# Optimization experiments

Measured on AMD Instinct MI355X. Metric: run time of the kernel, lower is better.

## Reference

```python
import jax, jax.numpy as jnp
import numpy as np

WIN = (7, 7)
NUM_HEADS = 6
DIM = 192
NW = 64          # windows per image
BATCH = 64       # images
B_ = BATCH * NW  # 4096 window-batches
N = WIN[0] * WIN[1]  # 49


def _relative_position_index():
    ch, cw = np.arange(WIN[0]), np.arange(WIN[1])
    coords = np.stack(np.meshgrid(ch, cw, indexing='ij'))          # [2, Wh, Ww]
    cf = coords.reshape(2, -1)                                      # [2, N]
    rel = cf[:, :, None] - cf[:, None, :]                           # [2, N, N]
    rel = rel.transpose(1, 2, 0).astype(np.int64)                   # [N, N, 2]
    rel[:, :, 0] += WIN[0] - 1
    rel[:, :, 1] += WIN[1] - 1
    rel[:, :, 0] *= 2 * WIN[1] - 1
    return rel.sum(-1).astype(np.int32)                             # [N, N]


def setup_inputs() -> dict:
    key = jax.random.key(0)
    ks = jax.random.split(key, 8)
    x = jax.random.normal(ks[0], (B_, N, DIM), dtype=jnp.float32)
    # additive shift-window mask: 0 where allowed, -100 where disallowed
    u = jax.random.uniform(ks[1], (NW, N, N))
    attn_mask = jnp.where(u < 0.15, -100.0, 0.0).astype(jnp.float32)
    rpb_table = jax.random.normal(ks[2], ((2 * WIN[0] - 1) * (2 * WIN[1] - 1), NUM_HEADS), dtype=jnp.float32) * 0.02
    rel_index = jnp.asarray(_relative_position_index())
    std = 1.0 / np.sqrt(DIM)
    qkv_w = jax.random.normal(ks[3], (3 * DIM, DIM), dtype=jnp.float32) * std
    qkv_b = jax.random.normal(ks[4], (3 * DIM,), dtype=jnp.float32) * 0.02
    proj_w = jax.random.normal(ks[5], (DIM, DIM), dtype=jnp.float32) * std
    proj_b = jax.random.normal(ks[6], (DIM,), dtype=jnp.float32) * 0.02
    return {"x": x, "attn_mask": attn_mask, "rpb_table": rpb_table,
            "rel_index": rel_index, "qkv_w": qkv_w, "qkv_b": qkv_b,
            "proj_w": proj_w, "proj_b": proj_b}


def reference(x, attn_mask, rpb_table, rel_index, qkv_w, qkv_b, proj_w, proj_b):
    Bw, n, C = x.shape
    H = NUM_HEADS
    hd = C // H
    scale = hd ** -0.5
    # qkv projection: [Bw, N, 3, H, hd] -> (3, Bw, H, N, hd)
    qkv = (x @ qkv_w.T + qkv_b).reshape(Bw, n, 3, H, hd).transpose(2, 0, 3, 1, 4)
    q, k, v = qkv[0], qkv[1], qkv[2]
    # gathered relative position bias: [H, N, N]
    rel_bias = rpb_table[rel_index.reshape(-1)].reshape(n, n, H).transpose(2, 0, 1)
    # scores [Bw, H, N, N]
    attn = jnp.einsum('bhnd,bhmd->bhnm', q * scale, k) + rel_bias[None]
    nW = attn_mask.shape[0]
    attn = attn.reshape(Bw // nW, nW, H, n, n) + attn_mask[None, :, None]
    attn = jax.nn.softmax(attn.reshape(Bw, H, n, n), axis=-1)
    out = jnp.einsum('bhnm,bhmd->bhnd', attn, v)  # [Bw, H, N, hd]
    out = out.transpose(0, 2, 1, 3).reshape(Bw, n, C)
    return out @ proj_w.T + proj_b
```

## Files before the change

### kernel.cpp

```cpp
#include <hip/hip_runtime.h>
#include <stdint.h>

typedef unsigned short ushort_t;
typedef __attribute__((ext_vector_type(8))) short bf16x8;
typedef __attribute__((ext_vector_type(4))) float f32x4;
typedef __attribute__((ext_vector_type(4))) unsigned int u32x4;

#define NTOK 49
#define DIMC 192
#define NH 6
#define HD 32
#define SCALE 0.17677669529663687f
#define XS 200
#define VTS 72
#define PS 72
#define MS 66
#define RS 68

#define OFF_X    0
#define OFF_Q    25600
#define OFF_K    51200
#define OFF_VT   76800
#define OFF_P    104448
#define OFF_MASK 122880
#define OFF_RPB  139776
#define OFF_REL  145184
#define OFF_BQ   153888
#define OFF_BP   156192
#define SMEM_BYTES 156960

#define QKVW_N (576 * 192)
#define PROJW_N (192 * 192)
#define QKV_GRP (4 * 9 * 6 * 64)
#define PROJ_GRP (4 * 3 * 6 * 64)
#define WBF_BYTES ((QKVW_N + PROJW_N) * 2)
#define BIAS_FLOATS (64 * 6 * 4 * 4 * 4 * 16 * 4)
#define WS_NEED1 ((size_t)WBF_BYTES)
#define WS_NEED2 ((size_t)WBF_BYTES + (size_t)BIAS_FLOATS * 4)

__device__ __forceinline__ ushort_t f2bf(float f) {
    uint32_t x = __builtin_bit_cast(uint32_t, f);
    x += 0x7fffu + ((x >> 16) & 1u);
    return (ushort_t)(x >> 16);
}

__device__ __forceinline__ bf16x8 cvt8(const float* p) {
    f32x4 a = *(const f32x4*)p;
    f32x4 b = *(const f32x4*)(p + 4);
    bf16x8 r;
    r[0] = (short)f2bf(a[0]); r[1] = (short)f2bf(a[1]);
    r[2] = (short)f2bf(a[2]); r[3] = (short)f2bf(a[3]);
    r[4] = (short)f2bf(b[0]); r[5] = (short)f2bf(b[1]);
    r[6] = (short)f2bf(b[2]); r[7] = (short)f2bf(b[3]);
    return r;
}

__global__ __launch_bounds__(256) void swz_weights_kernel(
    const float* __restrict__ qkvw, const float* __restrict__ projw,
    ushort_t* __restrict__ dst)
{
    int i = blockIdx.x * 256 + threadIdx.x;
    if (i >= QKV_GRP + PROJ_GRP) return;
    const float* src;
    float s = 1.0f;
    if (i < QKV_GRP) {
        int lane = i & 63, t = i >> 6;
        int kk = t % 6, nt = (t / 6) % 9, cq = t / 54;
        int col = cq * 144 + nt * 16 + (lane & 15);
        int k0 = kk * 32 + (lane >> 4) * 8;
        src = qkvw + col * DIMC + k0;
        if (col < 192) s = SCALE;
    } else {
        int j = i - QKV_GRP;
        int lane = j & 63, t = j >> 6;
        int kk = t % 6, nt = (t / 6) % 3, cq = t / 18;
        int col = cq * 48 + nt * 16 + (lane & 15);
        int k0 = kk * 32 + (lane >> 4) * 8;
        src = projw + col * DIMC + k0;
    }
    f32x4 a = *(const f32x4*)src;
    f32x4 b = *(const f32x4*)(src + 4);
    u32x4 o;
    o[0] = (uint32_t)f2bf(a[0] * s) | ((uint32_t)f2bf(a[1] * s) << 16);
    o[1] = (uint32_t)f2bf(a[2] * s) | ((uint32_t)f2bf(a[3] * s) << 16);
    o[2] = (uint32_t)f2bf(b[0] * s) | ((uint32_t)f2bf(b[1] * s) << 16);
    o[3] = (uint32_t)f2bf(b[2] * s) | ((uint32_t)f2bf(b[3] * s) << 16);
    *(u32x4*)(dst + (size_t)i * 8) = o;
}

__global__ __launch_bounds__(256) void bias_kernel(
    const float* __restrict__ mask_g, const float* __restrict__ rpb_g,
    const int* __restrict__ rel_g, float* __restrict__ dst)
{
    int i = blockIdx.x * 256 + threadIdx.x;
    if (i >= BIAS_FLOATS / 4) return;
    int c = i & 15, g = (i >> 4) & 3, t = (i >> 6) & 3, wsid = (i >> 8) & 3;
    int hw = i >> 10;
    int h = hw % 6, wi = hw / 6;
    int m0 = 16 * wsid + 4 * g, n = 16 * t + c;
    f32x4 v;
    #pragma unroll
    for (int r = 0; r < 4; ++r) {
        int m = m0 + r;
        float val;
        if (n >= NTOK)      val = -30000.0f;
        else if (m >= NTOK) val = 0.0f;
        else val = mask_g[(size_t)wi * (NTOK * NTOK) + m * NTOK + n]
                 + rpb_g[(size_t)rel_g[m * NTOK + n] * NH + h];
        v[r] = val;
    }
    *(f32x4*)(dst + (size_t)i * 4) = v;
}

template <int MODE>
__global__ __launch_bounds__(512, 2) void win_attn_kernel(
    const float* __restrict__ x_g,
    const float* __restrict__ mask_g,
    const float* __restrict__ rpb_g,
    const int* __restrict__ rel_g,
    const float* __restrict__ qkvw_g,
    const float* __restrict__ qkvb_g,
    const float* __restrict__ projw_g,
    const float* __restrict__ projb_g,
    const ushort_t* __restrict__ wbf_g,
    const float* __restrict__ bias_g,
    float* __restrict__ out_g)
{
    extern __shared__ char smem[];
    ushort_t* x_lds  = (ushort_t*)(smem + OFF_X);
    ushort_t* q_lds  = (ushort_t*)(smem + OFF_Q);
    ushort_t* k_lds  = (ushort_t*)(smem + OFF_K);
    ushort_t* vT     = (ushort_t*)(smem + OFF_VT);
    ushort_t* P_lds  = (ushort_t*)(smem + OFF_P);
    float*    mask_p = (float*)(smem + OFF_MASK);
    float*    rpb_l  = (float*)(smem + OFF_RPB);
    ushort_t* rel_p  = (ushort_t*)(smem + OFF_REL);
    float*    bq     = (float*)(smem + OFF_BQ);
    float*    bp     = (float*)(smem + OFF_BP);

    const int tid  = threadIdx.x;
    const int b    = blockIdx.x;
    const int wi   = b & 63;
    const int w    = tid >> 6;
    const int lane = tid & 63;
    const int g    = lane >> 4;
    const int c    = lane & 15;

    {
        const float* xg = x_g + (size_t)b * (NTOK * DIMC);
        for (int i = tid; i < 64 * 24; i += 512) {
            int row = i / 24, col = (i % 24) * 8;
            u32x4 v = {0u, 0u, 0u, 0u};
            if (row < NTOK) {
                const float* src = xg + row * DIMC + col;
                f32x4 a = *(const f32x4*)src;
                f32x4 d = *(const f32x4*)(src + 4);
                v[0] = (uint32_t)f2bf(a[0]) | ((uint32_t)f2bf(a[1]) << 16);
                v[1] = (uint32_t)f2bf(a[2]) | ((uint32_t)f2bf(a[3]) << 16);
                v[2] = (uint32_t)f2bf(d[0]) | ((uint32_t)f2bf(d[1]) << 16);
                v[3] = (uint32_t)f2bf(d[2]) | ((uint32_t)f2bf(d[3]) << 16);
            }
            *(u32x4*)&x_lds[row * XS + col] = v;
        }
        if constexpr (MODE < 2) {
            const float* mw = mask_g + (size_t)wi * (NTOK * NTOK);
            for (int i = tid; i < 64 * 64; i += 512) {
                int m = i >> 6, n = i & 63;
                float f;
                if (n >= NTOK)      f = -30000.0f;
                else if (m >= NTOK) f = 0.0f;
                else                f = mw[m * NTOK + n];
                mask_p[m * MS + n] = f;
                rel_p[m * RS + n] = (m < NTOK && n < NTOK) ? (ushort_t)rel_g[m * NTOK + n]
                                                           : (ushort_t)0;
            }
            for (int i = tid; i < 169 * 6; i += 512)
                rpb_l[(i / 6) * 8 + (i % 6)] = rpb_g[i];
        }
        for (int i = tid; i < 576; i += 512) {
            float v = qkvb_g[i];
            if constexpr (MODE == 2) { if (i < 192) v *= SCALE; }
            bq[i] = v;
        }
        if (tid < 192) bp[tid] = projb_g[tid];
    }
    __syncthreads();

    {
        const int mh = w >> 2, cq = w & 3;
        const ushort_t* wq = wbf_g + (size_t)cq * (9 * 6 * 64 * 8);

        bf16x8 ring[4][6];
        if constexpr (MODE >= 1) {
            #pragma unroll
            for (int p = 0; p < 3; ++p)
                #pragma unroll
                for (int kk = 0; kk < 6; ++kk)
                    ring[p][kk] = *(const bf16x8*)(wq + (size_t)((p * 6 + kk) * 64 + lane) * 8);
            __builtin_amdgcn_sched_barrier(0);
        }

        bf16x8 ax[2][6];
        #pragma unroll
        for (int mt = 0; mt < 2; ++mt)
            #pragma unroll
            for (int kk = 0; kk < 6; ++kk)
                ax[mt][kk] = *(const bf16x8*)&x_lds[(32 * mh + 16 * mt + c) * XS + kk * 32 + g * 8];

        #pragma unroll
        for (int nt = 0; nt < 9; ++nt) {
            const int cg = 144 * cq + nt * 16 + c;
            bf16x8 bw[6];
            if constexpr (MODE >= 1) {
                if (nt + 3 < 9) {
                    #pragma unroll
                    for (int kk = 0; kk < 6; ++kk)
                        ring[(nt + 3) & 3][kk] =
                            *(const bf16x8*)(wq + (size_t)(((nt + 3) * 6 + kk) * 64 + lane) * 8);
                }
                __builtin_amdgcn_sched_barrier(0);
                #pragma unroll
                for (int kk = 0; kk < 6; ++kk) bw[kk] = ring[nt & 3][kk];
            } else {
                #pragma unroll
                for (int kk = 0; kk < 6; ++kk)
                    bw[kk] = cvt8(qkvw_g + (size_t)cg * DIMC + kk * 32 + g * 8);
            }
            f32x4 z = {0.f, 0.f, 0.f, 0.f};
            f32x4 acc[2] = {z, z};
            #pragma unroll
            for (int kk = 0; kk < 6; ++kk)
                #pragma unroll
                for (int mt = 0; mt < 2; ++mt)
                    acc[mt] = __builtin_amdgcn_mfma_f32_16x16x32_bf16(ax[mt][kk], bw[kk], acc[mt], 0, 0, 0);

            const float bias = bq[cg];
            const int seg = 144 * cq + nt * 16;
            if (seg < 192) {
                #pragma unroll
                for (int mt = 0; mt < 2; ++mt)
                    #pragma unroll
                    for (int r = 0; r < 4; ++r)
                        q_lds[(32 * mh + 16 * mt + g * 4 + r) * XS + cg] = f2bf(acc[mt][r] + bias);
            } else if (seg < 384) {
                const int ck = cg - 192;
                #pragma unroll
                for (int mt = 0; mt < 2; ++mt)
                    #pragma unroll
                    for (int r = 0; r < 4; ++r)
                        k_lds[(32 * mh + 16 * mt + g * 4 + r) * XS + ck] = f2bf(acc[mt][r] + bias);
            } else {
                const int cv = cg - 384;
                #pragma unroll
                for (int mt = 0; mt < 2; ++mt) {
                    uint32_t lo = (uint32_t)f2bf(acc[mt][0] + bias) | ((uint32_t)f2bf(acc[mt][1] + bias) << 16);
                    uint32_t hi = (uint32_t)f2bf(acc[mt][2] + bias) | ((uint32_t)f2bf(acc[mt][3] + bias) << 16);
                    uint32_t* dst = (uint32_t*)&vT[cv * VTS + 32 * mh + 16 * mt + g * 4];
                    dst[0] = lo; dst[1] = hi;
                }
            }
        }
    }
    __syncthreads();

    bf16x8 pw[3][6];
    {
        const int wsid = w & 3, hh = w >> 2;
        ushort_t* Pw = P_lds + w * (16 * PS);
        const int mq0 = 16 * wsid + g * 4;

        auto head = [&](int h) {
            bf16x8 aq = *(const bf16x8*)&q_lds[(16 * wsid + c) * XS + h * HD + g * 8];
            f32x4 S[4];
            if constexpr (MODE == 2) {
                const float* bC = bias_g + ((size_t)((wi * 6 + h) * 4 + wsid) * 4) * 256 + lane * 4;
                #pragma unroll
                for (int t = 0; t < 4; ++t) {
                    f32x4 Ct = *(const f32x4*)(bC + t * 256);
                    bf16x8 bk = *(const bf16x8*)&k_lds[(16 * t + c) * XS + h * HD + g * 8];
                    S[t] = __builtin_amdgcn_mfma_f32_16x16x32_bf16(aq, bk, Ct, 0, 0, 0);
                }
            } else {
                #pragma unroll
                for (int t = 0; t < 4; ++t) {
                    bf16x8 bk = *(const bf16x8*)&k_lds[(16 * t + c) * XS + h * HD + g * 8];
                    f32x4 z = {0.f, 0.f, 0.f, 0.f};
                    S[t] = __builtin_amdgcn_mfma_f32_16x16x32_bf16(aq, bk, z, 0, 0, 0);
                }
            }
            float rinv[4];
            #pragma unroll
            for (int r = 0; r < 4; ++r) {
                float sv[4];
                if constexpr (MODE == 2) {
                    #pragma unroll
                    for (int t = 0; t < 4; ++t) sv[t] = S[t][r];
                } else {
                    const int mq = mq0 + r;
                    const float*    mrow = mask_p + mq * MS;
                    const ushort_t* rrow = rel_p + mq * RS;
                    #pragma unroll
                    for (int t = 0; t < 4; ++t) {
                        const int n = 16 * t + c;
                        sv[t] = S[t][r] * SCALE + rpb_l[(int)rrow[n] * 8 + h] + mrow[n];
                    }
                }
                float vmax = fmaxf(fmaxf(sv[0], sv[1]), fmaxf(sv[2], sv[3]));
                #pragma unroll
                for (int xm = 1; xm < 16; xm <<= 1)
                    vmax = fmaxf(vmax, __shfl_xor(vmax, xm));
                float sum = 0.f;
                float ev[4];
                #pragma unroll
                for (int t = 0; t < 4; ++t) {
                    ev[t] = __expf(fmaxf(sv[t] - vmax, -80.0f));
                    sum += ev[t];
                }
                #pragma unroll
                for (int xm = 1; xm < 16; xm <<= 1)
                    sum += __shfl_xor(sum, xm);
                rinv[r] = 1.0f / sum;
                #pragma unroll
                for (int t = 0; t < 4; ++t)
                    Pw[(g * 4 + r) * PS + 16 * t + c] = f2bf(ev[t]);
            }
            f32x4 z = {0.f, 0.f, 0.f, 0.f};
            f32x4 O[2] = {z, z};
            #pragma unroll
            for (int ks = 0; ks < 2; ++ks) {
                bf16x8 ap = *(const bf16x8*)&Pw[c * PS + ks * 32 + g * 8];
                #pragma unroll
                for (int nt = 0; nt < 2; ++nt) {
                    bf16x8 bv = *(const bf16x8*)&vT[(h * HD + nt * 16 + c) * VTS + ks * 32 + g * 8];
                    O[nt] = __builtin_amdgcn_mfma_f32_16x16x32_bf16(ap, bv, O[nt], 0, 0, 0);
                }
            }
            #pragma unroll
            for (int nt = 0; nt < 2; ++nt)
                #pragma unroll
                for (int r = 0; r < 4; ++r)
                    x_lds[(16 * wsid + g * 4 + r) * XS + h * HD + nt * 16 + c] =
                        f2bf(O[nt][r] * rinv[r]);
        };

        head(hh * 3 + 0);
        head(hh * 3 + 1);
        if constexpr (MODE >= 1) {
            const int cq4 = w & 3;
            const ushort_t* wp = wbf_g + QKVW_N + (size_t)cq4 * (3 * 6 * 64 * 8);
            #pragma unroll
            for (int nt = 0; nt < 3; ++nt)
                #pragma unroll
                for (int kk = 0; kk < 6; ++kk)
                    pw[nt][kk] = *(const bf16x8*)(wp + (size_t)((nt * 6 + kk) * 64 + lane) * 8);
            __builtin_amdgcn_sched_barrier(0);
        }
        head(hh * 3 + 2);
    }
    __syncthreads();

    {
        const int mh = w >> 2, cq4 = w & 3;
        bf16x8 aa[2][6];
        #pragma unroll
        for (int mt = 0; mt < 2; ++mt)
            #pragma unroll
            for (int kk = 0; kk < 6; ++kk)
                aa[mt][kk] = *(const bf16x8*)&x_lds[(32 * mh + 16 * mt + c) * XS + kk * 32 + g * 8];

        float* og = out_g + (size_t)b * (NTOK * DIMC);
        #pragma unroll
        for (int nt = 0; nt < 3; ++nt) {
            const int cg = 48 * cq4 + nt * 16 + c;
            bf16x8 bw[6];
            #pragma unroll
            for (int kk = 0; kk < 6; ++kk) {
                if constexpr (MODE >= 1)
                    bw[kk] = pw[nt][kk];
                else
                    bw[kk] = cvt8(projw_g + (size_t)cg * DIMC + kk * 32 + g * 8);
            }
            f32x4 z = {0.f, 0.f, 0.f, 0.f};
            f32x4 acc[2] = {z, z};
            #pragma unroll
            for (int kk = 0; kk < 6; ++kk)
                #pragma unroll
                for (int mt = 0; mt < 2; ++mt)
                    acc[mt] = __builtin_amdgcn_mfma_f32_16x16x32_bf16(aa[mt][kk], bw[kk], acc[mt], 0, 0, 0);
            const float bias = bp[cg];
            #pragma unroll
            for (int mt = 0; mt < 2; ++mt)
                #pragma unroll
                for (int r = 0; r < 4; ++r) {
                    const int row = 32 * mh + 16 * mt + g * 4 + r;
                    if (row < NTOK) og[row * DIMC + cg] = acc[mt][r] + bias;
                }
        }
    }
}

extern "C" void kernel_launch(void* const* d_in, const int* in_sizes, int n_in,
                              void* d_out, int out_size, void* d_ws, size_t ws_size,
                              hipStream_t stream) {
    (void)in_sizes; (void)n_in; (void)out_size;
    const float* x_g     = (const float*)d_in[0];
    const float* mask_g  = (const float*)d_in[1];
    const float* rpb_g   = (const float*)d_in[2];
    const int*   rel_g   = (const int*)d_in[3];
    const float* qkvw_g  = (const float*)d_in[4];
    const float* qkvb_g  = (const float*)d_in[5];
    const float* projw_g = (const float*)d_in[6];
    const float* projb_g = (const float*)d_in[7];
    float*       out_g   = (float*)d_out;

    const bool has_w = (d_ws != nullptr) && (ws_size >= WS_NEED1);
    const bool has_b = (d_ws != nullptr) && (ws_size >= WS_NEED2);
    ushort_t* wbf = (ushort_t*)d_ws;
    float* bias4 = (float*)((char*)d_ws + WBF_BYTES);

    if (has_w) {
        int ngrp = QKV_GRP + PROJ_GRP;
        hipLaunchKernelGGL(swz_weights_kernel, dim3((ngrp + 255) / 256), dim3(256), 0, stream,
                           qkvw_g, projw_g, wbf);
    }
    if (has_b) {
        int nthr = BIAS_FLOATS / 4;
        hipLaunchKernelGGL(bias_kernel, dim3((nthr + 255) / 256), dim3(256), 0, stream,
                           mask_g, rpb_g, rel_g, bias4);
        hipFuncSetAttribute((const void*)win_attn_kernel<2>,
                            hipFuncAttributeMaxDynamicSharedMemorySize, SMEM_BYTES);
        hipLaunchKernelGGL(win_attn_kernel<2>, dim3(4096), dim3(512), SMEM_BYTES, stream,
                           x_g, mask_g, rpb_g, rel_g, qkvw_g, qkvb_g, projw_g, projb_g,
                           wbf, bias4, out_g);
    } else if (has_w) {
        hipFuncSetAttribute((const void*)win_attn_kernel<1>,
                            hipFuncAttributeMaxDynamicSharedMemorySize, SMEM_BYTES);
        hipLaunchKernelGGL(win_attn_kernel<1>, dim3(4096), dim3(512), SMEM_BYTES, stream,
                           x_g, mask_g, rpb_g, rel_g, qkvw_g, qkvb_g, projw_g, projb_g,
                           wbf, (const float*)nullptr, out_g);
    } else {
        hipFuncSetAttribute((const void*)win_attn_kernel<0>,
                            hipFuncAttributeMaxDynamicSharedMemorySize, SMEM_BYTES);
        hipLaunchKernelGGL(win_attn_kernel<0>, dim3(4096), dim3(512), SMEM_BYTES, stream,
                           x_g, mask_g, rpb_g, rel_g, qkvw_g, qkvb_g, projw_g, projb_g,
                           (const ushort_t*)nullptr, (const float*)nullptr, out_g);
    }
}
```

Before: 249.9 us.

## Process two windows per block with prefetched next-window x in registers

Each block now handles two consecutive windows, with the grid halved. The second window's x is loaded into registers during the first window and written to a second LDS buffer after attention, so that load overlaps compute. Projection weights are loaded once and reused for both windows. Biases are folded into the MFMA accumulator init, and conversions use packed v_cvt_pk_bf16_f32. The cost is fewer blocks in flight, more register pressure, and an LDS region shared with mask/rpb buffers.

```diff
diff --git a/kernel.cpp b/kernel.cpp
--- a/kernel.cpp
+++ b/kernel.cpp
@@ -16,17 +16,19 @@
 #define PS 72
 #define MS 66
 #define RS 68
+#define NWIN 2
 
 #define OFF_X    0
 #define OFF_Q    25600
 #define OFF_K    51200
 #define OFF_VT   76800
 #define OFF_P    104448
-#define OFF_MASK 122880
-#define OFF_RPB  139776
-#define OFF_REL  145184
-#define OFF_BQ   153888
-#define OFF_BP   156192
+#define OFF_BQ   122880
+#define OFF_BP   125184
+#define OFF_X1   125952
+#define OFF_MASK 125952
+#define OFF_RPB  142848
+#define OFF_REL  148256
 #define SMEM_BYTES 156960
 
 #define QKVW_N (576 * 192)
@@ -42,6 +44,11 @@
     uint32_t x = __builtin_bit_cast(uint32_t, f);
     x += 0x7fffu + ((x >> 16) & 1u);
     return (ushort_t)(x >> 16);
+}
+__device__ __forceinline__ uint32_t cvtpk(float lo, float hi) {
+    uint32_t r;
+    asm("v_cvt_pk_bf16_f32 %0, %1, %2" : "=v"(r) : "v"(lo), "v"(hi));
+    return r;
 }
 
 __device__ __forceinline__ bf16x8 cvt8(const float* p) {
@@ -128,6 +135,7 @@
 {
     extern __shared__ char smem[];
     ushort_t* x_lds  = (ushort_t*)(smem + OFF_X);
+    ushort_t* x1_lds = (ushort_t*)(smem + OFF_X1);
     ushort_t* q_lds  = (ushort_t*)(smem + OFF_Q);
     ushort_t* k_lds  = (ushort_t*)(smem + OFF_K);
     ushort_t* vT     = (ushort_t*)(smem + OFF_VT);
@@ -139,15 +147,14 @@
     float*    bp     = (float*)(smem + OFF_BP);
 
     const int tid  = threadIdx.x;
-    const int b    = blockIdx.x;
-    const int wi   = b & 63;
+    const int blk  = blockIdx.x;
     const int w    = tid >> 6;
     const int lane = tid & 63;
     const int g    = lane >> 4;
     const int c    = lane & 15;
 
-    {
-        const float* xg = x_g + (size_t)b * (NTOK * DIMC);
+    auto stage_x = [&](int bb, ushort_t* dst) {
+        const float* xg = x_g + (size_t)bb * (NTOK * DIMC);
         for (int i = tid; i < 64 * 24; i += 512) {
             int row = i / 24, col = (i % 24) * 8;
             u32x4 v = {0u, 0u, 0u, 0u};
@@ -155,246 +162,308 @@
                 const float* src = xg + row * DIMC + col;
                 f32x4 a = *(const f32x4*)src;
                 f32x4 d = *(const f32x4*)(src + 4);
-                v[0] = (uint32_t)f2bf(a[0]) | ((uint32_t)f2bf(a[1]) << 16);
-                v[1] = (uint32_t)f2bf(a[2]) | ((uint32_t)f2bf(a[3]) << 16);
-                v[2] = (uint32_t)f2bf(d[0]) | ((uint32_t)f2bf(d[1]) << 16);
-                v[3] = (uint32_t)f2bf(d[2]) | ((uint32_t)f2bf(d[3]) << 16);
-            }
-            *(u32x4*)&x_lds[row * XS + col] = v;
+                v[0] = cvtpk(a[0], a[1]); v[1] = cvtpk(a[2], a[3]);
+                v[2] = cvtpk(d[0], d[1]); v[3] = cvtpk(d[2], d[3]);
+            }
+            *(u32x4*)&dst[row * XS + col] = v;
         }
-        if constexpr (MODE < 2) {
-            const float* mw = mask_g + (size_t)wi * (NTOK * NTOK);
-            for (int i = tid; i < 64 * 64; i += 512) {
-                int m = i >> 6, n = i & 63;
-                float f;
-                if (n >= NTOK)      f = -30000.0f;
-                else if (m >= NTOK) f = 0.0f;
-                else                f = mw[m * NTOK + n];
-                mask_p[m * MS + n] = f;
-                rel_p[m * RS + n] = (m < NTOK && n < NTOK) ? (ushort_t)rel_g[m * NTOK + n]
-                                                           : (ushort_t)0;
-            }
-            for (int i = tid; i < 169 * 6; i += 512)
-                rpb_l[(i / 6) * 8 + (i % 6)] = rpb_g[i];
+    };
+    auto stage_aux = [&](int wi) {
+        const float* mw = mask_g + (size_t)wi * (NTOK * NTOK);
+        for (int i = tid; i < 64 * 64; i += 512) {
+            int m = i >> 6, n = i & 63;
+            float f;
+            if (n >= NTOK)      f = -30000.0f;
+            else if (m >= NTOK) f = 0.0f;
+            else                f = mw[m * NTOK + n];
+            mask_p[m * MS + n] = f;
+            rel_p[m * RS + n] = (m < NTOK && n < NTOK) ? (ushort_t)rel_g[m * NTOK + n]
+                                                       : (ushort_t)0;
         }
-        for (int i = tid; i < 576; i += 512) {
-            float v = qkvb_g[i];
-            if constexpr (MODE == 2) { if (i < 192) v *= SCALE; }
-            bq[i] = v;
-        }
-        if (tid < 192) bp[tid] = projb_g[tid];
+        for (int i = tid; i < 169 * 6; i += 512)
+            rpb_l[(i / 6) * 8 + (i % 6)] = rpb_g[i];
+    };
+
+    stage_x(blk * NWIN, x_lds);
+    if constexpr (MODE < 2) stage_aux((blk * NWIN) & 63);
+    for (int i = tid; i < 576; i += 512) {
+        float v = qkvb_g[i];
+        if constexpr (MODE >= 1) { if (i < 192) v *= SCALE; }
+        bq[i] = v;
     }
+    if (tid < 192) bp[tid] = projb_g[tid];
     __syncthreads();
 
-    {
-        const int mh = w >> 2, cq = w & 3;
-        const ushort_t* wq = wbf_g + (size_t)cq * (9 * 6 * 64 * 8);
-
-        bf16x8 ring[4][6];
-        if constexpr (MODE >= 1) {
-            #pragma unroll
-            for (int p = 0; p < 3; ++p)
-                #pragma unroll
-                for (int kk = 0; kk < 6; ++kk)
-                    ring[p][kk] = *(const bf16x8*)(wq + (size_t)((p * 6 + kk) * 64 + lane) * 8);
-            __builtin_amdgcn_sched_barrier(0);
-        }
-
-        bf16x8 ax[2][6];
-        #pragma unroll
-        for (int mt = 0; mt < 2; ++mt)
-            #pragma unroll
-            for (int kk = 0; kk < 6; ++kk)
-                ax[mt][kk] = *(const bf16x8*)&x_lds[(32 * mh + 16 * mt + c) * XS + kk * 32 + g * 8];
-
-        #pragma unroll
-        for (int nt = 0; nt < 9; ++nt) {
-            const int cg = 144 * cq + nt * 16 + c;
-            bf16x8 bw[6];
+    bf16x8 pw[3][6];
+    f32x4 xa0, xa1, xa2, xd0, xd1, xd2;
+
+    #pragma unroll 1
+    for (int wdx = 0; wdx < NWIN; ++wdx) {
+        const int bb = blk * NWIN + wdx;
+        const int wi = bb & 63;
+        ushort_t* xb = (MODE == 2 && (wdx & 1)) ? x1_lds : x_lds;
+
+        {
+            const int mh = w >> 2, cq = w & 3;
+            const ushort_t* wq = wbf_g + (size_t)cq * (9 * 6 * 64 * 8);
+
+            bf16x8 ring[4][6];
             if constexpr (MODE >= 1) {
-                if (nt + 3 < 9) {
+                #pragma unroll
+                for (int p = 0; p < 3; ++p)
                     #pragma unroll
                     for (int kk = 0; kk < 6; ++kk)
-                        ring[(nt + 3) & 3][kk] =
-                            *(const bf16x8*)(wq + (size_t)(((nt + 3) * 6 + kk) * 64 + lane) * 8);
-                }
+                        ring[p][kk] = *(const bf16x8*)(wq + (size_t)((p * 6 + kk) * 64 + lane) * 8);
                 __builtin_amdgcn_sched_barrier(0);
-                #pragma unroll
-                for (int kk = 0; kk < 6; ++kk) bw[kk] = ring[nt & 3][kk];
-            } else {
-                #pragma unroll
-                for (int kk = 0; kk < 6; ++kk)
-                    bw[kk] = cvt8(qkvw_g + (size_t)cg * DIMC + kk * 32 + g * 8);
-            }
-            f32x4 z = {0.f, 0.f, 0.f, 0.f};
-            f32x4 acc[2] = {z, z};
-            #pragma unroll
-            for (int kk = 0; kk < 6; ++kk)
-                #pragma unroll
-                for (int mt = 0; mt < 2; ++mt)
-                    acc[mt] = __builtin_amdgcn_mfma_f32_16x16x32_bf16(ax[mt][kk], bw[kk], acc[mt], 0, 0, 0);
-
-            const float bias = bq[cg];
-            const int seg = 144 * cq + nt * 16;
-            if (seg < 192) {
-                #pragma unroll
-                for (int mt = 0; mt < 2; ++mt)
-                    #pragma unroll
-                    for (int r = 0; r < 4; ++r)
-                        q_lds[(32 * mh + 16 * mt + g * 4 + r) * XS + cg] = f2bf(acc[mt][r] + bias);
-            } else if (seg < 384) {
-                const int ck = cg - 192;
-                #pragma unroll
-                for (int mt = 0; mt < 2; ++mt)
-                    #pragma unroll
-                    for (int r = 0; r < 4; ++r)
-                        k_lds[(32 * mh + 16 * mt + g * 4 + r) * XS + ck] = f2bf(acc[mt][r] + bias);
-            } else {
-                const int cv = cg - 384;
-                #pragma unroll
-                for (int mt = 0; mt < 2; ++mt) {
-                    uint32_t lo = (uint32_t)f2bf(acc[mt][0] + bias) | ((uint32_t)f2bf(acc[mt][1] + bias) << 16);
-                    uint32_t hi = (uint32_t)f2bf(acc[mt][2] + bias) | ((uint32_t)f2bf(acc[mt][3] + bias) << 16);
-                    uint32_t* dst = (uint32_t*)&vT[cv * VTS + 32 * mh + 16 * mt + g * 4];
-                    dst[0] = lo; dst[1] = hi;
-                }
-            }
-        }
-    }
-    __syncthreads();
-
-    bf16x8 pw[3][6];
-    {
-        const int wsid = w & 3, hh = w >> 2;
-        ushort_t* Pw = P_lds + w * (16 * PS);
-        const int mq0 = 16 * wsid + g * 4;
-
-        auto head = [&](int h) {
-            bf16x8 aq = *(const bf16x8*)&q_lds[(16 * wsid + c) * XS + h * HD + g * 8];
-            f32x4 S[4];
-            if constexpr (MODE == 2) {
-                const float* bC = bias_g + ((size_t)((wi * 6 + h) * 4 + wsid) * 4) * 256 + lane * 4;
-                #pragma unroll
-                for (int t = 0; t < 4; ++t) {
-                    f32x4 Ct = *(const f32x4*)(bC + t * 256);
-                    bf16x8 bk = *(const bf16x8*)&k_lds[(16 * t + c) * XS + h * HD + g * 8];
-                    S[t] = __builtin_amdgcn_mfma_f32_16x16x32_bf16(aq, bk, Ct, 0, 0, 0);
-                }
-            } else {
-                #pragma unroll
-                for (int t = 0; t < 4; ++t) {
-                    bf16x8 bk = *(const bf16x8*)&k_lds[(16 * t + c) * XS + h * HD + g * 8];
-                    f32x4 z = {0.f, 0.f, 0.f, 0.f};
-                    S[t] = __builtin_amdgcn_mfma_f32_16x16x32_bf16(aq, bk, z, 0, 0, 0);
-                }
-            }
-            float rinv[4];
-            #pragma unroll
-            for (int r = 0; r < 4; ++r) {
-                float sv[4];
-                if constexpr (MODE == 2) {
-                    #pragma unroll
-                    for (int t = 0; t < 4; ++t) sv[t] = S[t][r];
-                } else {
-                    const int mq = mq0 + r;
-                    const float*    mrow = mask_p + mq * MS;
-                    const ushort_t* rrow = rel_p + mq * RS;
-                    #pragma unroll
-                    for (int t = 0; t < 4; ++t) {
-                        const int n = 16 * t + c;
-                        sv[t] = S[t][r] * SCALE + rpb_l[(int)rrow[n] * 8 + h] + mrow[n];
-                    }
-                }
-                float vmax = fmaxf(fmaxf(sv[0], sv[1]), fmaxf(sv[2], sv[3]));
-                #pragma unroll
-                for (int xm = 1; xm < 16; xm <<= 1)
-                    vmax = fmaxf(vmax, __shfl_xor(vmax, xm));
-                float sum = 0.f;
-                float ev[4];
-                #pragma unroll
-                for (int t = 0; t < 4; ++t) {
-                    ev[t] = __expf(fmaxf(sv[t] - vmax, -80.0f));
-                    sum += ev[t];
-                }
-                #pragma unroll
-                for (int xm = 1; xm < 16; xm <<= 1)
-                    sum += __shfl_xor(sum, xm);
-                rinv[r] = 1.0f / sum;
-                #pragma unroll
-                for (int t = 0; t < 4; ++t)
-                    Pw[(g * 4 + r) * PS + 16 * t + c] = f2bf(ev[t]);
-            }
-            f32x4 z = {0.f, 0.f, 0.f, 0.f};
-            f32x4 O[2] = {z, z};
-            #pragma unroll
-            for (int ks = 0; ks < 2; ++ks) {
-                bf16x8 ap = *(const bf16x8*)&Pw[c * PS + ks * 32 + g * 8];
-                #pragma unroll
-                for (int nt = 0; nt < 2; ++nt) {
-                    bf16x8 bv = *(const bf16x8*)&vT[(h * HD + nt * 16 + c) * VTS + ks * 32 + g * 8];
-                    O[nt] = __builtin_amdgcn_mfma_f32_16x16x32_bf16(ap, bv, O[nt], 0, 0, 0);
-                }
-            }
-            #pragma unroll
-            for (int nt = 0; nt < 2; ++nt)
-                #pragma unroll
-                for (int r = 0; r < 4; ++r)
-                    x_lds[(16 * wsid + g * 4 + r) * XS + h * HD + nt * 16 + c] =
-                        f2bf(O[nt][r] * rinv[r]);
-        };
-
-        head(hh * 3 + 0);
-        head(hh * 3 + 1);
-        if constexpr (MODE >= 1) {
-            const int cq4 = w & 3;
-            const ushort_t* wp = wbf_g + QKVW_N + (size_t)cq4 * (3 * 6 * 64 * 8);
-            #pragma unroll
-            for (int nt = 0; nt < 3; ++nt)
-                #pragma unroll
-                for (int kk = 0; kk < 6; ++kk)
-                    pw[nt][kk] = *(const bf16x8*)(wp + (size_t)((nt * 6 + kk) * 64 + lane) * 8);
-            __builtin_amdgcn_sched_barrier(0);
-        }
-        head(hh * 3 + 2);
-    }
-    __syncthreads();
-
-    {
-        const int mh = w >> 2, cq4 = w & 3;
-        bf16x8 aa[2][6];
-        #pragma unroll
-        for (int mt = 0; mt < 2; ++mt)
-            #pragma unroll
-            for (int kk = 0; kk < 6; ++kk)
-                aa[mt][kk] = *(const bf16x8*)&x_lds[(32 * mh + 16 * mt + c) * XS + kk * 32 + g * 8];
-
-        float* og = out_g + (size_t)b * (NTOK * DIMC);
-        #pragma unroll
-        for (int nt = 0; nt < 3; ++nt) {
-            const int cg = 48 * cq4 + nt * 16 + c;
-            bf16x8 bw[6];
-            #pragma unroll
-            for (int kk = 0; kk < 6; ++kk) {
-                if constexpr (MODE >= 1)
-                    bw[kk] = pw[nt][kk];
-                else
-                    bw[kk] = cvt8(projw_g + (size_t)cg * DIMC + kk * 32 + g * 8);
-            }
-            f32x4 z = {0.f, 0.f, 0.f, 0.f};
-            f32x4 acc[2] = {z, z};
-            #pragma unroll
-            for (int kk = 0; kk < 6; ++kk)
-                #pragma unroll
-                for (int mt = 0; mt < 2; ++mt)
-                    acc[mt] = __builtin_amdgcn_mfma_f32_16x16x32_bf16(aa[mt][kk], bw[kk], acc[mt], 0, 0, 0);
-            const float bias = bp[cg];
+            }
+
+            bf16x8 ax[2][6];
             #pragma unroll
             for (int mt = 0; mt < 2; ++mt)
                 #pragma unroll
+                for (int kk = 0; kk < 6; ++kk)
+                    ax[mt][kk] = *(const bf16x8*)&xb[(32 * mh + 16 * mt + c) * XS + kk * 32 + g * 8];
+
+            #pragma unroll
+            for (int nt = 0; nt < 9; ++nt) {
+                const int cg = 144 * cq + nt * 16 + c;
+                bf16x8 bw[6];
+                if constexpr (MODE >= 1) {
+                    if (nt + 3 < 9) {
+                        #pragma unroll
+                        for (int kk = 0; kk < 6; ++kk)
+                            ring[(nt + 3) & 3][kk] =
+                                *(const bf16x8*)(wq + (size_t)(((nt + 3) * 6 + kk) * 64 + lane) * 8);
+                    }
+                    __builtin_amdgcn_sched_barrier(0);
+                    #pragma unroll
+                    for (int kk = 0; kk < 6; ++kk) bw[kk] = ring[nt & 3][kk];
+                } else {
+                    #pragma unroll
+                    for (int kk = 0; kk < 6; ++kk)
+                        bw[kk] = cvt8(qkvw_g + (size_t)cg * DIMC + kk * 32 + g * 8);
+                }
+                const float bias = bq[cg];
+                f32x4 acc[2];
+                acc[0] = (f32x4){bias, bias, bias, bias};
+                acc[1] = acc[0];
+                #pragma unroll
+                for (int kk = 0; kk < 6; ++kk)
+                    #pragma unroll
+                    for (int mt = 0; mt < 2; ++mt)
+                        acc[mt] = __builtin_amdgcn_mfma_f32_16x16x32_bf16(ax[mt][kk], bw[kk], acc[mt], 0, 0, 0);
+
+                const int seg = 144 * cq + nt * 16;
+                if (seg < 192) {
+                    #pragma unroll
+                    for (int mt = 0; mt < 2; ++mt) {
+                        uint32_t p01 = cvtpk(acc[mt][0], acc[mt][1]);
+                        uint32_t p23 = cvtpk(acc[mt][2], acc[mt][3]);
+                        const int r0 = 32 * mh + 16 * mt + g * 4;
+                        q_lds[(r0 + 0) * XS + cg] = (ushort_t)p01;
+                        q_lds[(r0 + 1) * XS + cg] = (ushort_t)(p01 >> 16);
+                        q_lds[(r0 + 2) * XS + cg] = (ushort_t)p23;
+                        q_lds[(r0 + 3) * XS + cg] = (ushort_t)(p23 >> 16);
+                    }
+                } else if (seg < 384) {
+                    const int ck = cg - 192;
+                    #pragma unroll
+                    for (int mt = 0; mt < 2; ++mt) {
+                        uint32_t p01 = cvtpk(acc[mt][0], acc[mt][1]);
+                        uint32_t p23 = cvtpk(acc[mt][2], acc[mt][3]);
+                        const int r0 = 32 * mh + 16 * mt + g * 4;
+                        k_lds[(r0 + 0) * XS + ck] = (ushort_t)p01;
+                        k_lds[(r0 + 1) * XS + ck] = (ushort_t)(p01 >> 16);
+                        k_lds[(r0 + 2) * XS + ck] = (ushort_t)p23;
+                        k_lds[(r0 + 3) * XS + ck] = (ushort_t)(p23 >> 16);
+                    }
+                } else {
+                    const int cv = cg - 384;
+                    #pragma unroll
+                    for (int mt = 0; mt < 2; ++mt) {
+                        uint32_t* dst = (uint32_t*)&vT[cv * VTS + 32 * mh + 16 * mt + g * 4];
+                        dst[0] = cvtpk(acc[mt][0], acc[mt][1]);
+                        dst[1] = cvtpk(acc[mt][2], acc[mt][3]);
+                    }
+                }
+            }
+        }
+        __syncthreads();
+
+        {
+            const int wsid = w & 3, hh = w >> 2;
+            ushort_t* Pw = P_lds + w * (16 * PS);
+            const int mq0 = 16 * wsid + g * 4;
+
+            if (MODE == 2 && wdx == 0) {
+                const float* xg1 = x_g + (size_t)(bb + 1) * (NTOK * DIMC);
+                f32x4 z = {0.f, 0.f, 0.f, 0.f};
+                xa0 = xa1 = xa2 = xd0 = xd1 = xd2 = z;
+                {
+                    int i0 = tid;            int r0 = i0 / 24, c0 = (i0 % 24) * 8;
+                    int i1 = tid + 512;      int r1 = i1 / 24, c1 = (i1 % 24) * 8;
+                    int i2 = tid + 1024;     int r2 = i2 / 24, c2 = (i2 % 24) * 8;
+                    if (r0 < NTOK) { xa0 = *(const f32x4*)(xg1 + r0 * DIMC + c0); xd0 = *(const f32x4*)(xg1 + r0 * DIMC + c0 + 4); }
+                    if (r1 < NTOK) { xa1 = *(const f32x4*)(xg1 + r1 * DIMC + c1); xd1 = *(const f32x4*)(xg1 + r1 * DIMC + c1 + 4); }
+                    if (r2 < NTOK) { xa2 = *(const f32x4*)(xg1 + r2 * DIMC + c2); xd2 = *(const f32x4*)(xg1 + r2 * DIMC + c2 + 4); }
+                }
+                __builtin_amdgcn_sched_barrier(0);
+            }
+
+            auto head = [&](int h) {
+                bf16x8 aq = *(const bf16x8*)&q_lds[(16 * wsid + c) * XS + h * HD + g * 8];
+                f32x4 S[4];
+                if constexpr (MODE == 2) {
+                    const float* bC = bias_g + ((size_t)((wi * 6 + h) * 4 + wsid) * 4) * 256 + lane * 4;
+                    #pragma unroll
+                    for (int t = 0; t < 4; ++t) {
+                        f32x4 Ct = *(const f32x4*)(bC + t * 256);
+                        bf16x8 bk = *(const bf16x8*)&k_lds[(16 * t + c) * XS + h * HD + g * 8];
+                        S[t] = __builtin_amdgcn_mfma_f32_16x16x32_bf16(aq, bk, Ct, 0, 0, 0);
+                    }
+                } else {
+                    #pragma unroll
+                    for (int t = 0; t < 4; ++t) {
+                        bf16x8 bk = *(const bf16x8*)&k_lds[(16 * t + c) * XS + h * HD + g * 8];
+                        f32x4 z = {0.f, 0.f, 0.f, 0.f};
+                        S[t] = __builtin_amdgcn_mfma_f32_16x16x32_bf16(aq, bk, z, 0, 0, 0);
+                    }
+                }
+                float rinv[4];
+                #pragma unroll
                 for (int r = 0; r < 4; ++r) {
-                    const int row = 32 * mh + 16 * mt + g * 4 + r;
-                    if (row < NTOK) og[row * DIMC + cg] = acc[mt][r] + bias;
-                }
+                    float sv[4];
+                    if constexpr (MODE == 2) {
+                        #pragma unroll
+                        for (int t = 0; t < 4; ++t) sv[t] = S[t][r];
+                    } else {
+                        const int mq = mq0 + r;
+                        const float*    mrow = mask_p + mq * MS;
+                        const ushort_t* rrow = rel_p + mq * RS;
+                        #pragma unroll
+                        for (int t = 0; t < 4; ++t) {
+                            const int n = 16 * t + c;
+                            float sc = (MODE == 0) ? SCALE : 1.0f;
+                            sv[t] = S[t][r] * sc + rpb_l[(int)rrow[n] * 8 + h] + mrow[n];
+                        }
+                    }
+                    float vmax = fmaxf(fmaxf(sv[0], sv[1]), fmaxf(sv[2], sv[3]));
+                    #pragma unroll
+                    for (int xm = 1; xm < 16; xm <<= 1)
+                        vmax = fmaxf(vmax, __shfl_xor(vmax, xm));
+                    float sum = 0.f;
+                    float ev[4];
+                    #pragma unroll
+                    for (int t = 0; t < 4; ++t) {
+                        ev[t] = __expf(fmaxf(sv[t] - vmax, -80.0f));
+                        sum += ev[t];
+                    }
+                    #pragma unroll
+                    for (int xm = 1; xm < 16; xm <<= 1)
+                        sum += __shfl_xor(sum, xm);
+                    rinv[r] = 1.0f / sum;
+                    uint32_t p01 = cvtpk(ev[0], ev[1]);
+                    uint32_t p23 = cvtpk(ev[2], ev[3]);
+                    ushort_t* pr = Pw + (g * 4 + r) * PS + c;
+                    pr[0]  = (ushort_t)p01;
+                    pr[16] = (ushort_t)(p01 >> 16);
+                    pr[32] = (ushort_t)p23;
+                    pr[48] = (ushort_t)(p23 >> 16);
+                }
+                f32x4 z = {0.f, 0.f, 0.f, 0.f};
+                f32x4 O[2] = {z, z};
+                #pragma unroll
+                for (int ks = 0; ks < 2; ++ks) {
+                    bf16x8 ap = *(const bf16x8*)&Pw[c * PS + ks * 32 + g * 8];
+                    #pragma unroll
+                    for (int nt = 0; nt < 2; ++nt) {
+                        bf16x8 bv = *(const bf16x8*)&vT[(h * HD + nt * 16 + c) * VTS + ks * 32 + g * 8];
+                        O[nt] = __builtin_amdgcn_mfma_f32_16x16x32_bf16(ap, bv, O[nt], 0, 0, 0);
+                    }
+                }
+                #pragma unroll
+                for (int r = 0; r < 4; ++r) {
+                    uint32_t po = cvtpk(O[0][r] * rinv[r], O[1][r] * rinv[r]);
+                    ushort_t* ar = xb + (16 * wsid + g * 4 + r) * XS + h * HD + c;
+                    ar[0]  = (ushort_t)po;
+                    ar[16] = (ushort_t)(po >> 16);
+                }
+            };
+
+            head(hh * 3 + 0);
+            head(hh * 3 + 1);
+            if (MODE >= 1 && wdx == 0) {
+                const int cq4 = w & 3;
+                const ushort_t* wp = wbf_g + QKVW_N + (size_t)cq4 * (3 * 6 * 64 * 8);
+                #pragma unroll
+                for (int nt = 0; nt < 3; ++nt)
+                    #pragma unroll
+                    for (int kk = 0; kk < 6; ++kk)
+                        pw[nt][kk] = *(const bf16x8*)(wp + (size_t)((nt * 6 + kk) * 64 + lane) * 8);
+                __builtin_amdgcn_sched_barrier(0);
+            }
+            head(hh * 3 + 2);
+
+            if (MODE == 2 && wdx == 0) {
+                int i0 = tid;        int r0 = i0 / 24, c0 = (i0 % 24) * 8;
+                int i1 = tid + 512;  int r1 = i1 / 24, c1 = (i1 % 24) * 8;
+                int i2 = tid + 1024; int r2 = i2 / 24, c2 = (i2 % 24) * 8;
+                u32x4 v0 = {cvtpk(xa0[0], xa0[1]), cvtpk(xa0[2], xa0[3]), cvtpk(xd0[0], xd0[1]), cvtpk(xd0[2], xd0[3])};
+                u32x4 v1 = {cvtpk(xa1[0], xa1[1]), cvtpk(xa1[2], xa1[3]), cvtpk(xd1[0], xd1[1]), cvtpk(xd1[2], xd1[3])};
+                u32x4 v2 = {cvtpk(xa2[0], xa2[1]), cvtpk(xa2[2], xa2[3]), cvtpk(xd2[0], xd2[1]), cvtpk(xd2[2], xd2[3])};
+                *(u32x4*)&x1_lds[r0 * XS + c0] = v0;
+                *(u32x4*)&x1_lds[r1 * XS + c1] = v1;
+                *(u32x4*)&x1_lds[r2 * XS + c2] = v2;
+            }
+        }
+        __syncthreads();
+
+        {
+            const int mh = w >> 2, cq4 = w & 3;
+            bf16x8 aa[2][6];
+            #pragma unroll
+            for (int mt = 0; mt < 2; ++mt)
+                #pragma unroll
+                for (int kk = 0; kk < 6; ++kk)
+                    aa[mt][kk] = *(const bf16x8*)&xb[(32 * mh + 16 * mt + c) * XS + kk * 32 + g * 8];
+
+            float* og = out_g + (size_t)bb * (NTOK * DIMC);
+            #pragma unroll
+            for (int nt = 0; nt < 3; ++nt) {
+                const int cg = 48 * cq4 + nt * 16 + c;
+                bf16x8 bw[6];
+                #pragma unroll
+                for (int kk = 0; kk < 6; ++kk) {
+                    if constexpr (MODE >= 1)
+                        bw[kk] = pw[nt][kk];
+                    else
+                        bw[kk] = cvt8(projw_g + (size_t)cg * DIMC + kk * 32 + g * 8);
+                }
+                const float bias = bp[cg];
+                f32x4 acc[2];
+                acc[0] = (f32x4){bias, bias, bias, bias};
+                acc[1] = acc[0];
+                #pragma unroll
+                for (int kk = 0; kk < 6; ++kk)
+                    #pragma unroll
+                    for (int mt = 0; mt < 2; ++mt)
+                        acc[mt] = __builtin_amdgcn_mfma_f32_16x16x32_bf16(aa[mt][kk], bw[kk], acc[mt], 0, 0, 0);
+                #pragma unroll
+                for (int mt = 0; mt < 2; ++mt)
+                    #pragma unroll
+                    for (int r = 0; r < 4; ++r) {
+                        const int row = 32 * mh + 16 * mt + g * 4 + r;
+                        if (row < NTOK) og[row * DIMC + cg] = acc[mt][r];
+                    }
+            }
+        }
+        if (wdx + 1 < NWIN) {
+            if constexpr (MODE < 2) {
+                __syncthreads();
+                stage_x(bb + 1, x_lds);
+                stage_aux((bb + 1) & 63);
+                __syncthreads();
+            }
         }
     }
 }
@@ -429,19 +498,19 @@
                            mask_g, rpb_g, rel_g, bias4);
         hipFuncSetAttribute((const void*)win_attn_kernel<2>,
                             hipFuncAttributeMaxDynamicSharedMemorySize, SMEM_BYTES);
-        hipLaunchKernelGGL(win_attn_kernel<2>, dim3(4096), dim3(512), SMEM_BYTES, stream,
+        hipLaunchKernelGGL(win_attn_kernel<2>, dim3(2048), dim3(512), SMEM_BYTES, stream,
                            x_g, mask_g, rpb_g, rel_g, qkvw_g, qkvb_g, projw_g, projb_g,
                            wbf, bias4, out_g);
     } else if (has_w) {
         hipFuncSetAttribute((const void*)win_attn_kernel<1>,
                             hipFuncAttributeMaxDynamicSharedMemorySize, SMEM_BYTES);
-        hipLaunchKernelGGL(win_attn_kernel<1>, dim3(4096), dim3(512), SMEM_BYTES, stream,
+        hipLaunchKernelGGL(win_attn_kernel<1>, dim3(2048), dim3(512), SMEM_BYTES, stream,
                            x_g, mask_g, rpb_g, rel_g, qkvw_g, qkvb_g, projw_g, projb_g,
                            wbf, (const float*)nullptr, out_g);
     } else {
         hipFuncSetAttribute((const void*)win_attn_kernel<0>,
                             hipFuncAttributeMaxDynamicSharedMemorySize, SMEM_BYTES);
-        hipLaunchKernelGGL(win_attn_kernel<0>, dim3(4096), dim3(512), SMEM_BYTES, stream,
+        hipLaunchKernelGGL(win_attn_kernel<0>, dim3(2048), dim3(512), SMEM_BYTES, stream,
                            x_g, mask_g, rpb_g, rel_g, qkvw_g, qkvb_g, projw_g, projb_g,
                            (const ushort_t*)nullptr, (const float*)nullptr, out_g);
     }
```

New measurement: 815.7 us. 3.26x slower.
